# Kernel tuning notes

Measured on AMD Instinct MI355X. Metric: run time of the kernel, lower is better.

## Reference

```python
import jax, jax.numpy as jnp
import numpy as np

N_HEAD = 16
D_MODEL = 1024
HEAD_DIM = D_MODEL // N_HEAD
B, S = 2, 2048


def setup_inputs() -> dict:
    key = jax.random.key(0)
    ks = jax.random.split(key, 7)
    qry = jax.random.normal(ks[0], (B, S, D_MODEL), dtype=jnp.float32)
    k_in = jax.random.normal(ks[1], (B, S, D_MODEL), dtype=jnp.float32)
    v_in = jax.random.normal(ks[2], (B, S, D_MODEL), dtype=jnp.float32)
    # causal boolean mask (B, S_q, S_k) as asserted in SelfAttention.forward
    attn_mask = jnp.broadcast_to(jnp.tril(jnp.ones((S, S), dtype=bool)), (B, S, S))
    scale = 1.0 / np.sqrt(D_MODEL)
    Wq = jax.random.normal(ks[3], (D_MODEL, D_MODEL), dtype=jnp.float32) * scale
    Wk = jax.random.normal(ks[4], (D_MODEL, D_MODEL), dtype=jnp.float32) * scale
    Wv = jax.random.normal(ks[5], (D_MODEL, D_MODEL), dtype=jnp.float32) * scale
    Wo = jax.random.normal(ks[6], (D_MODEL, D_MODEL), dtype=jnp.float32) * scale
    return {"qry": qry, "key": k_in, "val": v_in, "attn_mask": attn_mask,
            "Wq": Wq, "Wk": Wk, "Wv": Wv, "Wo": Wo}


def reference(qry, key, val, attn_mask, Wq, Wk, Wv, Wo):
    Bq, Sq, _ = qry.shape
    # torch Linear: y = x @ W.T (no bias)
    q = (qry @ Wq.T).reshape(Bq, Sq, N_HEAD, HEAD_DIM).transpose(0, 2, 1, 3)
    k = (key @ Wk.T).reshape(Bq, -1, N_HEAD, HEAD_DIM).transpose(0, 2, 1, 3)
    v = (val @ Wv.T).reshape(Bq, -1, N_HEAD, HEAD_DIM).transpose(0, 2, 1, 3)
    # scores: [B, H, Sq, Sk]
    scores = jnp.einsum('bhqd,bhkd->bhqk', q, k) / jnp.sqrt(jnp.float32(HEAD_DIM * N_HEAD) / N_HEAD)
    # attn_bias: 0 where mask True, -inf where False; broadcast over heads
    bias = jnp.where(attn_mask[:, None, :, :], 0.0, -jnp.inf).astype(scores.dtype)
    attn_weights = jax.nn.softmax(scores + bias, axis=-1)
    attn_feats = jnp.einsum('bhqk,bhkd->bhqd', attn_weights, v)
    attn_feats = attn_feats.transpose(0, 2, 1, 3).reshape(Bq, Sq, D_MODEL)
    output = attn_feats @ Wo.T
    return output, attn_weights
```

## Files before the change

kernel.cpp:

```cpp
#include <hip/hip_runtime.h>
#include <hip/hip_bf16.h>
#include <cstdint>
#include <cstddef>

#define DM 1024
#define NH 16
#define HD 64
#define BB 2
#define SS 2048

typedef __attribute__((ext_vector_type(4))) float f32x4;
typedef __attribute__((ext_vector_type(8))) short bf16x8;

typedef __attribute__((address_space(1))) const void GV;
typedef __attribute__((address_space(3))) void LV;

#define WAITV(N) asm volatile("s_waitcnt vmcnt(" N ")" ::: "memory")
#define SBAR do { __builtin_amdgcn_s_barrier(); asm volatile("" ::: "memory"); } while (0)

__global__ __launch_bounds__(256) void cvt_all(
    const float* s0, const float* s1, const float* s2, const float* s3,
    const float* s4, const float* s5, const float* s6,
    __hip_bfloat16* d0, __hip_bfloat16* d1, __hip_bfloat16* d2, __hip_bfloat16* d3,
    __hip_bfloat16* d4, __hip_bfloat16* d5, __hip_bfloat16* d6) {
    const float* s; __hip_bfloat16* d; int n4;
    switch (blockIdx.y) {
        case 0: s = s0; d = d0; n4 = 1 << 20; break;
        case 1: s = s1; d = d1; n4 = 1 << 20; break;
        case 2: s = s2; d = d2; n4 = 1 << 20; break;
        case 3: s = s3; d = d3; n4 = 1 << 18; break;
        case 4: s = s4; d = d4; n4 = 1 << 18; break;
        case 5: s = s5; d = d5; n4 = 1 << 18; break;
        default: s = s6; d = d6; n4 = 1 << 18; break;
    }
    for (int i = blockIdx.x * 256 + threadIdx.x; i < n4; i += 1024 * 256) {
        float4 v = reinterpret_cast<const float4*>(s)[i];
        ushort4 o;
        o.x = __builtin_bit_cast(unsigned short, __float2bfloat16(v.x));
        o.y = __builtin_bit_cast(unsigned short, __float2bfloat16(v.y));
        o.z = __builtin_bit_cast(unsigned short, __float2bfloat16(v.z));
        o.w = __builtin_bit_cast(unsigned short, __float2bfloat16(v.w));
        reinterpret_cast<ushort4*>(d)[i] = o;
    }
}

template <typename OutT>
__device__ __forceinline__ void gemm_body(const __hip_bfloat16* __restrict__ A,
                                          const __hip_bfloat16* __restrict__ Bw,
                                          OutT* __restrict__ C, int M, int N, int K,
                                          float alpha,
                                          __hip_bfloat16* As, __hip_bfloat16* Bs) {
    const int lane = threadIdx.x & 63;
    const int wv = threadIdx.x >> 6;
    const int wr = wv >> 1, wc = wv & 1;
    const int g = lane >> 4, cq = lane & 15;
    const int tM = blockIdx.y * 128, tN = blockIdx.x * 128;

    f32x4 acc[4][4];
#pragma unroll
    for (int i = 0; i < 4; ++i)
#pragma unroll
        for (int j = 0; j < 4; ++j) acc[i][j] = (f32x4){0.f, 0.f, 0.f, 0.f};

    for (int k0 = 0; k0 < K; k0 += 32) {
        __syncthreads();
#pragma unroll
        for (int r = 0; r < 2; ++r) {
            int chunk = r * 256 + wv * 64 + lane;
            int row = chunk >> 2;
            int kk = (chunk & 3) * 8;
            __builtin_amdgcn_global_load_lds((GV*)(A + (size_t)(tM + row) * K + k0 + kk),
                                             (LV*)(As + (size_t)(r * 256 + wv * 64) * 8), 16, 0, 0);
            __builtin_amdgcn_global_load_lds((GV*)(Bw + (size_t)(tN + row) * K + k0 + kk),
                                             (LV*)(Bs + (size_t)(r * 256 + wv * 64) * 8), 16, 0, 0);
        }
        __syncthreads();

        bf16x8 af[4], bfr[4];
#pragma unroll
        for (int i = 0; i < 4; ++i)
            af[i] = *reinterpret_cast<const bf16x8*>(As + (wr * 64 + i * 16 + cq) * 32 + g * 8);
#pragma unroll
        for (int j = 0; j < 4; ++j)
            bfr[j] = *reinterpret_cast<const bf16x8*>(Bs + (wc * 64 + j * 16 + cq) * 32 + g * 8);
#pragma unroll
        for (int i = 0; i < 4; ++i)
#pragma unroll
            for (int j = 0; j < 4; ++j)
                acc[i][j] = __builtin_amdgcn_mfma_f32_16x16x32_bf16(af[i], bfr[j], acc[i][j], 0, 0, 0);
    }

#pragma unroll
    for (int i = 0; i < 4; ++i)
#pragma unroll
        for (int j = 0; j < 4; ++j)
#pragma unroll
            for (int rr = 0; rr < 4; ++rr) {
                int row = tM + wr * 64 + i * 16 + g * 4 + rr;
                int col = tN + wc * 64 + j * 16 + cq;
                float v = acc[i][j][rr] * alpha;
                if constexpr (__is_same(OutT, float)) {
                    C[(size_t)row * N + col] = v;
                } else {
                    C[(size_t)row * N + col] = __float2bfloat16(v);
                }
            }
}

#define QALPHA 0.1803368801111204f

__global__ __launch_bounds__(256) void gemm_qkv(
    const __hip_bfloat16* qa, const __hip_bfloat16* ka, const __hip_bfloat16* va,
    const __hip_bfloat16* wq, const __hip_bfloat16* wk, const __hip_bfloat16* wv,
    __hip_bfloat16* Qm, __hip_bfloat16* Km, __hip_bfloat16* Vm) {
    __shared__ __hip_bfloat16 As[128 * 32];
    __shared__ __hip_bfloat16 Bs[128 * 32];
    const __hip_bfloat16 *A, *Bw;
    __hip_bfloat16* C;
    float alpha = 1.0f;
    switch (blockIdx.z) {
        case 0: A = qa; Bw = wq; C = Qm; alpha = QALPHA; break;
        case 1: A = ka; Bw = wk; C = Km; break;
        default: A = va; Bw = wv; C = Vm; break;
    }
    gemm_body<__hip_bfloat16>(A, Bw, C, BB * SS, DM, DM, alpha, As, Bs);
}

__global__ __launch_bounds__(256) void gemm_out(const __hip_bfloat16* __restrict__ A,
                                                const __hip_bfloat16* __restrict__ Bw,
                                                float* __restrict__ C) {
    __shared__ __hip_bfloat16 As[128 * 32];
    __shared__ __hip_bfloat16 Bs[128 * 32];
    gemm_body<float>(A, Bw, C, BB * SS, DM, DM, 1.0f, As, Bs);
}

__global__ __launch_bounds__(256) void transpose_v(const __hip_bfloat16* __restrict__ V,
                                                   __hip_bfloat16* __restrict__ VT) {
    const int bh = blockIdx.x;
    const int b = bh >> 4, h = bh & 15;
    const int k0 = blockIdx.y * 64;
    __shared__ __hip_bfloat16 tile[64][68];
    const int r = threadIdx.x >> 4;
    const int c4 = threadIdx.x & 15;
#pragma unroll
    for (int rr = r; rr < 64; rr += 16) {
        ushort4 u = *reinterpret_cast<const ushort4*>(
            V + (size_t)(b * SS + k0 + rr) * DM + h * HD + c4 * 4);
        *reinterpret_cast<ushort4*>(&tile[rr][c4 * 4]) = u;
    }
    __syncthreads();
#pragma unroll
    for (int dd = r; dd < 64; dd += 16) {
        ushort4 o;
        o.x = __builtin_bit_cast(unsigned short, tile[c4 * 4 + 0][dd]);
        o.y = __builtin_bit_cast(unsigned short, tile[c4 * 4 + 1][dd]);
        o.z = __builtin_bit_cast(unsigned short, tile[c4 * 4 + 2][dd]);
        o.w = __builtin_bit_cast(unsigned short, tile[c4 * 4 + 3][dd]);
        *reinterpret_cast<ushort4*>(VT + ((size_t)bh * HD + dd) * SS + k0 + c4 * 4) = o;
    }
}

__global__ __launch_bounds__(256) void attn_fused(const __hip_bfloat16* __restrict__ Q,
                                                  const __hip_bfloat16* __restrict__ Kb,
                                                  const __hip_bfloat16* __restrict__ VT,
                                                  float* __restrict__ Wout,
                                                  __hip_bfloat16* __restrict__ feats) {
    __shared__ __hip_bfloat16 sbuf[4][64 * 64];
    __shared__ __hip_bfloat16 plds[4][16][64];
    const int idx = blockIdx.x;
    const int c = idx & 255, k = idx >> 8;
    const int bh = c >> 3;
    const int j = c & 7;
    const int qt = (k & 1) ? (31 - 2 * j - (k >> 1)) : (2 * j + (k >> 1));
    const int b = bh >> 4, h = bh & 15;
    const int lane = threadIdx.x & 63;
    const int wv = threadIdx.x >> 6;
    const int g = lane >> 4, cq = lane & 15;
    const int q0w = qt * 64 + wv * 16;
    const size_t rowbase = (size_t)b * SS;
    const int tmaxw = q0w >> 4;

    const __hip_bfloat16* qp = Q + (rowbase + q0w + cq) * DM + h * HD + g * 8;
    const bf16x8 qf0 = *reinterpret_cast<const bf16x8*>(qp);
    const bf16x8 qf1 = *reinterpret_cast<const bf16x8*>(qp + 32);

    auto stageK = [&](int kc, __hip_bfloat16* dst) {
#pragma unroll
        for (int i = 0; i < 2; ++i) {
            int slot = i * 256 + wv * 64 + lane;
            int row = slot >> 3, c16 = slot & 7;
            const __hip_bfloat16* src =
                Kb + (rowbase + kc * 64 + row) * DM + h * HD + ((c16 ^ (row & 7)) << 3);
            __builtin_amdgcn_global_load_lds(
                (GV*)src, (LV*)(dst + (size_t)(i * 256 + wv * 64) * 8), 16, 0, 0);
        }
    };
    auto stageV = [&](int kc, __hip_bfloat16* dst) {
#pragma unroll
        for (int i = 0; i < 2; ++i) {
            int slot = i * 256 + wv * 64 + lane;
            int row = slot >> 3, c16 = slot & 7;
            const __hip_bfloat16* src =
                VT + ((size_t)bh * HD + row) * SS + kc * 64 + ((c16 ^ (row & 7)) << 3);
            __builtin_amdgcn_global_load_lds(
                (GV*)src, (LV*)(dst + (size_t)(i * 256 + wv * 64) * 8), 16, 0, 0);
        }
    };

    const int swx = cq & 7;

    float l_[4] = {0.f, 0.f, 0.f, 0.f};
    stageK(0, sbuf[0]);
    stageK(qt < 1 ? qt : 1, sbuf[1]);
    stageK(qt < 2 ? qt : 2, sbuf[2]);
    WAITV("4");
    SBAR;
    for (int kc = 0; kc <= qt; ++kc) {
        const int nx = kc + 3;
        stageK(nx > qt ? qt : nx, sbuf[nx & 3]);
        const __hip_bfloat16* kbase = sbuf[kc & 3];
#pragma unroll
        for (int hh = 0; hh < 4; ++hh) {
            const int kt = kc * 4 + hh;
            if (kt > tmaxw) break;
            const __hip_bfloat16* kb = kbase + (hh * 16 + cq) * 64;
            bf16x8 kf0 = *reinterpret_cast<const bf16x8*>(kb + ((g ^ swx) << 3));
            bf16x8 kf1 = *reinterpret_cast<const bf16x8*>(kb + (((4 + g) ^ swx) << 3));
            f32x4 sc = (f32x4){0.f, 0.f, 0.f, 0.f};
            sc = __builtin_amdgcn_mfma_f32_16x16x32_bf16(qf0, kf0, sc, 0, 0, 0);
            sc = __builtin_amdgcn_mfma_f32_16x16x32_bf16(qf1, kf1, sc, 0, 0, 0);
            const int kk = kt * 16 + cq;
#pragma unroll
            for (int r = 0; r < 4; ++r) {
                const int qr = q0w + g * 4 + r;
                l_[r] += (kk <= qr) ? __builtin_amdgcn_exp2f(sc[r]) : 0.0f;
            }
        }
        if (kc < qt) {
            WAITV("4");
            SBAR;
        }
    }
    float invl[4];
#pragma unroll
    for (int r = 0; r < 4; ++r) {
        float l = l_[r];
#pragma unroll
        for (int mk = 1; mk < 16; mk <<= 1) l += __shfl_xor(l, mk);
        invl[r] = __builtin_amdgcn_rcpf(l);
    }

    f32x4 oacc[4];
#pragma unroll
    for (int j2 = 0; j2 < 4; ++j2) oacc[j2] = (f32x4){0.f, 0.f, 0.f, 0.f};

    SBAR;
    stageK(0, sbuf[0]);
    stageV(0, sbuf[2]);
    WAITV("0");
    SBAR;
    for (int kc = 0; kc <= qt; ++kc) {
        const int nx = kc + 1;
        const int nc = nx > qt ? qt : nx;
        stageK(nc, sbuf[nx & 1]);
        stageV(nc, sbuf[2 + (nx & 1)]);
        const __hip_bfloat16* kbase = sbuf[kc & 1];
        const __hip_bfloat16* vbase = sbuf[2 + (kc & 1)];

#pragma unroll
        for (int hh = 0; hh < 4; ++hh) {
            const int kt = kc * 4 + hh;
            if (kt <= tmaxw) {
                const __hip_bfloat16* kb = kbase + (hh * 16 + cq) * 64;
                bf16x8 kf0 = *reinterpret_cast<const bf16x8*>(kb + ((g ^ swx) << 3));
                bf16x8 kf1 = *reinterpret_cast<const bf16x8*>(kb + (((4 + g) ^ swx) << 3));
                f32x4 sc = (f32x4){0.f, 0.f, 0.f, 0.f};
                sc = __builtin_amdgcn_mfma_f32_16x16x32_bf16(qf0, kf0, sc, 0, 0, 0);
                sc = __builtin_amdgcn_mfma_f32_16x16x32_bf16(qf1, kf1, sc, 0, 0, 0);
                const int kk = kt * 16 + cq;
#pragma unroll
                for (int r = 0; r < 4; ++r) {
                    const int row = g * 4 + r;
                    const int qr = q0w + row;
                    float w = (kk <= qr) ? __builtin_amdgcn_exp2f(sc[r]) * invl[r] : 0.0f;
                    plds[wv][row][(hh * 16 + cq) ^ (8 * (row & 7))] = __float2bfloat16(w);
                }
            } else {
#pragma unroll
                for (int r = 0; r < 4; ++r) {
                    const int row = g * 4 + r;
                    plds[wv][row][(hh * 16 + cq) ^ (8 * (row & 7))] = __float2bfloat16(0.0f);
                }
            }
        }

        const int sw = 8 * swx;
        bf16x8 wa0 = *reinterpret_cast<const bf16x8*>(&plds[wv][cq][(g * 8) ^ sw]);
        bf16x8 wa1 = *reinterpret_cast<const bf16x8*>(&plds[wv][cq][(32 + g * 8) ^ sw]);
        __builtin_amdgcn_s_setprio(1);
#pragma unroll
        for (int j2 = 0; j2 < 4; ++j2) {
            const __hip_bfloat16* vb = vbase + (j2 * 16 + cq) * 64;
            bf16x8 vb0 = *reinterpret_cast<const bf16x8*>(vb + ((g ^ swx) << 3));
            bf16x8 vb1 = *reinterpret_cast<const bf16x8*>(vb + (((4 + g) ^ swx) << 3));
            oacc[j2] = __builtin_amdgcn_mfma_f32_16x16x32_bf16(wa0, vb0, oacc[j2], 0, 0, 0);
            oacc[j2] = __builtin_amdgcn_mfma_f32_16x16x32_bf16(wa1, vb1, oacc[j2], 0, 0, 0);
        }
        __builtin_amdgcn_s_setprio(0);

#pragma unroll
        for (int it = 0; it < 4; ++it) {
            const int row = it * 4 + g;
            ushort4 u = *reinterpret_cast<const ushort4*>(
                &plds[wv][row][(cq * 4) ^ (8 * (row & 7))]);
            f32x4 v4;
            v4[0] = __builtin_bit_cast(float, (uint32_t)u.x << 16);
            v4[1] = __builtin_bit_cast(float, (uint32_t)u.y << 16);
            v4[2] = __builtin_bit_cast(float, (uint32_t)u.z << 16);
            v4[3] = __builtin_bit_cast(float, (uint32_t)u.w << 16);
            __builtin_nontemporal_store(
                v4, reinterpret_cast<f32x4*>(
                        Wout + ((size_t)bh * SS + q0w + row) * SS + kc * 64 + cq * 4));
        }

        if (kc < qt) {
            WAITV("4");
            SBAR;
        }
    }

    const int zstart = (qt + 1) * 64;
    const f32x4 z4 = (f32x4){0.f, 0.f, 0.f, 0.f};
    for (int row = 0; row < 16; ++row) {
        float* rp = Wout + ((size_t)bh * SS + q0w + row) * SS;
        for (int cc = zstart + lane * 4; cc < SS; cc += 256)
            __builtin_nontemporal_store(z4, reinterpret_cast<f32x4*>(rp + cc));
    }

#pragma unroll
    for (int j2 = 0; j2 < 4; ++j2)
#pragma unroll
        for (int r = 0; r < 4; ++r)
            feats[(rowbase + q0w + g * 4 + r) * DM + h * HD + j2 * 16 + cq] =
                __float2bfloat16(oacc[j2][r]);
}

extern "C" void kernel_launch(void* const* d_in, const int* in_sizes, int n_in,
                              void* d_out, int out_size, void* d_ws, size_t ws_size,
                              hipStream_t stream) {
    (void)in_sizes; (void)n_in; (void)out_size;
    const float* qry = (const float*)d_in[0];
    const float* key = (const float*)d_in[1];
    const float* val = (const float*)d_in[2];
    const float* Wq = (const float*)d_in[4];
    const float* Wk = (const float*)d_in[5];
    const float* Wv = (const float*)d_in[6];
    const float* Wo = (const float*)d_in[7];

    float* out = (float*)d_out;
    float* w_out = out + (size_t)BB * SS * DM;

    const size_t E = (size_t)BB * SS * DM;
    const size_t W = (size_t)DM * DM;
    if (ws_size < (8 * E + 4 * W) * sizeof(__hip_bfloat16)) return;

    __hip_bfloat16* ws = (__hip_bfloat16*)d_ws;
    __hip_bfloat16* qb    = ws;
    __hip_bfloat16* kb    = ws + E;
    __hip_bfloat16* vb    = ws + 2 * E;
    __hip_bfloat16* wqb   = ws + 3 * E;
    __hip_bfloat16* wkb   = ws + 3 * E + W;
    __hip_bfloat16* wvb   = ws + 3 * E + 2 * W;
    __hip_bfloat16* wob   = ws + 3 * E + 3 * W;
    __hip_bfloat16* Qm    = ws + 3 * E + 4 * W;
    __hip_bfloat16* Km    = ws + 4 * E + 4 * W;
    __hip_bfloat16* Vm    = ws + 5 * E + 4 * W;
    __hip_bfloat16* VTm   = ws + 6 * E + 4 * W;
    __hip_bfloat16* feats = ws + 7 * E + 4 * W;

    cvt_all<<<dim3(1024, 7), 256, 0, stream>>>(qry, key, val, Wq, Wk, Wv, Wo,
                                               qb, kb, vb, wqb, wkb, wvb, wob);

    gemm_qkv<<<dim3(DM / 128, (BB * SS) / 128, 3), 256, 0, stream>>>(
        qb, kb, vb, wqb, wkb, wvb, Qm, Km, Vm);

    transpose_v<<<dim3(BB * NH, SS / 64), 256, 0, stream>>>(Vm, VTm);

    attn_fused<<<dim3(1024), 256, 0, stream>>>(Qm, Km, VTm, w_out, feats);

    gemm_out<<<dim3(DM / 128, (BB * SS) / 128), 256, 0, stream>>>(feats, wob, out);
}
```

Measured before the change: 241.1 us.

## Split softmax row-sum pass into separate kernel co-scheduled with V transpose

The first pass of attention, which computes the exp row sums and reciprocal normalizer for each query row, moves out of attn_fused into a new kernel. That kernel also performs the V transpose in its first 1024 blocks. The reciprocals go to a float buffer that reuses the no-longer-needed bf16 query workspace, and attn_fused loads them at the start. The aim is to overlap the transpose with the row-sum work and shorten the main attention kernel, at the cost of an extra global write and read of the normalizers and a kernel boundary.

```diff
diff --git a/kernel.cpp b/kernel.cpp
--- a/kernel.cpp
+++ b/kernel.cpp
@@ -134,35 +134,112 @@
     gemm_body<float>(A, Bw, C, BB * SS, DM, DM, 1.0f, As, Bs);
 }
 
-__global__ __launch_bounds__(256) void transpose_v(const __hip_bfloat16* __restrict__ V,
-                                                   __hip_bfloat16* __restrict__ VT) {
-    const int bh = blockIdx.x;
+__global__ __launch_bounds__(256) void tr_lpass(const __hip_bfloat16* __restrict__ V,
+                                                __hip_bfloat16* __restrict__ VT,
+                                                const __hip_bfloat16* __restrict__ Q,
+                                                const __hip_bfloat16* __restrict__ Kb,
+                                                float* __restrict__ linv) {
+    __shared__ __hip_bfloat16 smem[4][64 * 64];
+    const int idx = blockIdx.x;
+    if (idx < 1024) {
+        const int bh = idx >> 5;
+        const int b = bh >> 4, h = bh & 15;
+        const int k0 = (idx & 31) * 64;
+        __hip_bfloat16 (*tile)[68] = reinterpret_cast<__hip_bfloat16 (*)[68]>(&smem[0][0]);
+        const int r = threadIdx.x >> 4;
+        const int c4 = threadIdx.x & 15;
+#pragma unroll
+        for (int rr = r; rr < 64; rr += 16) {
+            ushort4 u = *reinterpret_cast<const ushort4*>(
+                V + (size_t)(b * SS + k0 + rr) * DM + h * HD + c4 * 4);
+            *reinterpret_cast<ushort4*>(&tile[rr][c4 * 4]) = u;
+        }
+        __syncthreads();
+#pragma unroll
+        for (int dd = r; dd < 64; dd += 16) {
+            ushort4 o;
+            o.x = __builtin_bit_cast(unsigned short, tile[c4 * 4 + 0][dd]);
+            o.y = __builtin_bit_cast(unsigned short, tile[c4 * 4 + 1][dd]);
+            o.z = __builtin_bit_cast(unsigned short, tile[c4 * 4 + 2][dd]);
+            o.w = __builtin_bit_cast(unsigned short, tile[c4 * 4 + 3][dd]);
+            *reinterpret_cast<ushort4*>(VT + ((size_t)bh * HD + dd) * SS + k0 + c4 * 4) = o;
+        }
+        return;
+    }
+    const int c = (idx - 1024) & 255, k = (idx - 1024) >> 8;
+    const int bh = c >> 3;
+    const int j = c & 7;
+    const int qt = (k & 1) ? (31 - 2 * j - (k >> 1)) : (2 * j + (k >> 1));
     const int b = bh >> 4, h = bh & 15;
-    const int k0 = blockIdx.y * 64;
-    __shared__ __hip_bfloat16 tile[64][68];
-    const int r = threadIdx.x >> 4;
-    const int c4 = threadIdx.x & 15;
-#pragma unroll
-    for (int rr = r; rr < 64; rr += 16) {
-        ushort4 u = *reinterpret_cast<const ushort4*>(
-            V + (size_t)(b * SS + k0 + rr) * DM + h * HD + c4 * 4);
-        *reinterpret_cast<ushort4*>(&tile[rr][c4 * 4]) = u;
-    }
-    __syncthreads();
-#pragma unroll
-    for (int dd = r; dd < 64; dd += 16) {
-        ushort4 o;
-        o.x = __builtin_bit_cast(unsigned short, tile[c4 * 4 + 0][dd]);
-        o.y = __builtin_bit_cast(unsigned short, tile[c4 * 4 + 1][dd]);
-        o.z = __builtin_bit_cast(unsigned short, tile[c4 * 4 + 2][dd]);
-        o.w = __builtin_bit_cast(unsigned short, tile[c4 * 4 + 3][dd]);
-        *reinterpret_cast<ushort4*>(VT + ((size_t)bh * HD + dd) * SS + k0 + c4 * 4) = o;
+    const int lane = threadIdx.x & 63;
+    const int wv = threadIdx.x >> 6;
+    const int g = lane >> 4, cq = lane & 15;
+    const int q0w = qt * 64 + wv * 16;
+    const size_t rowbase = (size_t)b * SS;
+    const int tmaxw = q0w >> 4;
+    const int swx = cq & 7;
+
+    const __hip_bfloat16* qp = Q + (rowbase + q0w + cq) * DM + h * HD + g * 8;
+    const bf16x8 qf0 = *reinterpret_cast<const bf16x8*>(qp);
+    const bf16x8 qf1 = *reinterpret_cast<const bf16x8*>(qp + 32);
+
+    auto stageK = [&](int kc, __hip_bfloat16* dst) {
+#pragma unroll
+        for (int i = 0; i < 2; ++i) {
+            int slot = i * 256 + wv * 64 + lane;
+            int row = slot >> 3, c16 = slot & 7;
+            const __hip_bfloat16* src =
+                Kb + (rowbase + kc * 64 + row) * DM + h * HD + ((c16 ^ (row & 7)) << 3);
+            __builtin_amdgcn_global_load_lds(
+                (GV*)src, (LV*)(dst + (size_t)(i * 256 + wv * 64) * 8), 16, 0, 0);
+        }
+    };
+
+    float l_[4] = {0.f, 0.f, 0.f, 0.f};
+    stageK(0, smem[0]);
+    stageK(qt < 1 ? qt : 1, smem[1]);
+    stageK(qt < 2 ? qt : 2, smem[2]);
+    WAITV("4");
+    SBAR;
+    for (int kc = 0; kc <= qt; ++kc) {
+        const int nx = kc + 3;
+        stageK(nx > qt ? qt : nx, smem[nx & 3]);
+        const __hip_bfloat16* kbase = smem[kc & 3];
+#pragma unroll
+        for (int hh = 0; hh < 4; ++hh) {
+            const int kt = kc * 4 + hh;
+            if (kt > tmaxw) break;
+            const __hip_bfloat16* kb = kbase + (hh * 16 + cq) * 64;
+            bf16x8 kf0 = *reinterpret_cast<const bf16x8*>(kb + ((g ^ swx) << 3));
+            bf16x8 kf1 = *reinterpret_cast<const bf16x8*>(kb + (((4 + g) ^ swx) << 3));
+            f32x4 sc = (f32x4){0.f, 0.f, 0.f, 0.f};
+            sc = __builtin_amdgcn_mfma_f32_16x16x32_bf16(qf0, kf0, sc, 0, 0, 0);
+            sc = __builtin_amdgcn_mfma_f32_16x16x32_bf16(qf1, kf1, sc, 0, 0, 0);
+            const int kk = kt * 16 + cq;
+#pragma unroll
+            for (int r = 0; r < 4; ++r) {
+                const int qr = q0w + g * 4 + r;
+                l_[r] += (kk <= qr) ? __builtin_amdgcn_exp2f(sc[r]) : 0.0f;
+            }
+        }
+        if (kc < qt) {
+            WAITV("4");
+            SBAR;
+        }
+    }
+#pragma unroll
+    for (int r = 0; r < 4; ++r) {
+        float l = l_[r];
+#pragma unroll
+        for (int mk = 1; mk < 16; mk <<= 1) l += __shfl_xor(l, mk);
+        if (cq == 0) linv[(size_t)bh * SS + q0w + g * 4 + r] = __builtin_amdgcn_rcpf(l);
     }
 }
 
 __global__ __launch_bounds__(256) void attn_fused(const __hip_bfloat16* __restrict__ Q,
                                                   const __hip_bfloat16* __restrict__ Kb,
                                                   const __hip_bfloat16* __restrict__ VT,
+                                                  const float* __restrict__ linv,
                                                   float* __restrict__ Wout,
                                                   __hip_bfloat16* __restrict__ feats) {
     __shared__ __hip_bfloat16 sbuf[4][64 * 64];
@@ -179,10 +256,15 @@
     const int q0w = qt * 64 + wv * 16;
     const size_t rowbase = (size_t)b * SS;
     const int tmaxw = q0w >> 4;
+    const int swx = cq & 7;
 
     const __hip_bfloat16* qp = Q + (rowbase + q0w + cq) * DM + h * HD + g * 8;
     const bf16x8 qf0 = *reinterpret_cast<const bf16x8*>(qp);
     const bf16x8 qf1 = *reinterpret_cast<const bf16x8*>(qp + 32);
+
+    float invl[4];
+#pragma unroll
+    for (int r = 0; r < 4; ++r) invl[r] = linv[(size_t)bh * SS + q0w + g * 4 + r];
 
     auto stageK = [&](int kc, __hip_bfloat16* dst) {
 #pragma unroll
@@ -207,54 +289,10 @@
         }
     };
 
-    const int swx = cq & 7;
-
-    float l_[4] = {0.f, 0.f, 0.f, 0.f};
-    stageK(0, sbuf[0]);
-    stageK(qt < 1 ? qt : 1, sbuf[1]);
-    stageK(qt < 2 ? qt : 2, sbuf[2]);
-    WAITV("4");
-    SBAR;
-    for (int kc = 0; kc <= qt; ++kc) {
-        const int nx = kc + 3;
-        stageK(nx > qt ? qt : nx, sbuf[nx & 3]);
-        const __hip_bfloat16* kbase = sbuf[kc & 3];
-#pragma unroll
-        for (int hh = 0; hh < 4; ++hh) {
-            const int kt = kc * 4 + hh;
-            if (kt > tmaxw) break;
-            const __hip_bfloat16* kb = kbase + (hh * 16 + cq) * 64;
-            bf16x8 kf0 = *reinterpret_cast<const bf16x8*>(kb + ((g ^ swx) << 3));
-            bf16x8 kf1 = *reinterpret_cast<const bf16x8*>(kb + (((4 + g) ^ swx) << 3));
-            f32x4 sc = (f32x4){0.f, 0.f, 0.f, 0.f};
-            sc = __builtin_amdgcn_mfma_f32_16x16x32_bf16(qf0, kf0, sc, 0, 0, 0);
-            sc = __builtin_amdgcn_mfma_f32_16x16x32_bf16(qf1, kf1, sc, 0, 0, 0);
-            const int kk = kt * 16 + cq;
-#pragma unroll
-            for (int r = 0; r < 4; ++r) {
-                const int qr = q0w + g * 4 + r;
-                l_[r] += (kk <= qr) ? __builtin_amdgcn_exp2f(sc[r]) : 0.0f;
-            }
-        }
-        if (kc < qt) {
-            WAITV("4");
-            SBAR;
-        }
-    }
-    float invl[4];
-#pragma unroll
-    for (int r = 0; r < 4; ++r) {
-        float l = l_[r];
-#pragma unroll
-        for (int mk = 1; mk < 16; mk <<= 1) l += __shfl_xor(l, mk);
-        invl[r] = __builtin_amdgcn_rcpf(l);
-    }
-
     f32x4 oacc[4];
 #pragma unroll
     for (int j2 = 0; j2 < 4; ++j2) oacc[j2] = (f32x4){0.f, 0.f, 0.f, 0.f};
 
-    SBAR;
     stageK(0, sbuf[0]);
     stageV(0, sbuf[2]);
     WAITV("0");
@@ -377,6 +415,7 @@
     __hip_bfloat16* Vm    = ws + 5 * E + 4 * W;
     __hip_bfloat16* VTm   = ws + 6 * E + 4 * W;
     __hip_bfloat16* feats = ws + 7 * E + 4 * W;
+    float* linv = (float*)qb;
 
     cvt_all<<<dim3(1024, 7), 256, 0, stream>>>(qry, key, val, Wq, Wk, Wv, Wo,
                                                qb, kb, vb, wqb, wkb, wvb, wob);
@@ -384,9 +423,9 @@
     gemm_qkv<<<dim3(DM / 128, (BB * SS) / 128, 3), 256, 0, stream>>>(
         qb, kb, vb, wqb, wkb, wvb, Qm, Km, Vm);
 
-    transpose_v<<<dim3(BB * NH, SS / 64), 256, 0, stream>>>(Vm, VTm);
-
-    attn_fused<<<dim3(1024), 256, 0, stream>>>(Qm, Km, VTm, w_out, feats);
+    tr_lpass<<<dim3(2048), 256, 0, stream>>>(Vm, VTm, Qm, Km, linv);
+
+    attn_fused<<<dim3(1024), 256, 0, stream>>>(Qm, Km, VTm, linv, w_out, feats);
 
     gemm_out<<<dim3(DM / 128, (BB * SS) / 128), 256, 0, stream>>>(feats, wob, out);
 }
```

Measured after the change: 254.8 us. 1.06x slower.
